# Optimization experiments

Hardware: AMD Instinct MI355X
Metric: run time of the kernel (lower is better)

The kernel has to match this reference:

```python
import jax, jax.numpy as jnp
import numpy as np

K, B, DA = 32, 16384, 128

def setup_inputs() -> dict:
    key = jax.random.key(0)
    ks = jax.random.split(key, 8)
    return {
        "x": jax.random.normal(ks[0], (B, DA), dtype=jnp.float32),
        "neigh_effect": jax.random.uniform(ks[1], (K, B), dtype=jnp.float32),
        "neigh_transform": jax.random.normal(ks[2], (K, B, DA), dtype=jnp.float32),
        "n_param": jax.random.uniform(ks[3], (DA,), dtype=jnp.float32),
        "ew": jax.random.normal(ks[4], (DA,), dtype=jnp.float32) * 0.1,
        "eb": jax.random.normal(ks[5], (1,), dtype=jnp.float32),
        "tw": jax.random.uniform(ks[6], (DA,), dtype=jnp.float32),
        "tb": jax.random.uniform(ks[7], (DA,), dtype=jnp.float32),
    }

def reference(x, neigh_effect, neigh_transform, n_param, ew, eb, tw, tb):
    # x: [B, da] (only used when no neighbors; here K>0 so neighbor path taken)
    k, b = neigh_effect.shape
    da = x.shape[1]
    # softmax over neighbor axis (dim=0 in torch)
    w = jax.nn.softmax(neigh_effect, axis=0)                    # [K, B]
    # faithful to torch reshape trick: x_[i].reshape(da, -1) * w[i], reshape back to (B, da)
    t = neigh_transform.reshape(k, da, b) * w[:, None, :]       # [K, da, B]
    x_sum = t.reshape(k, b, da).sum(axis=0)                     # [B, da]
    x_ = n_param * x_sum                                        # [B, da]
    effect = jax.nn.sigmoid(x_ @ ew + eb)[:, None]              # [B, 1] (Linear(da,1))
    transform = tw * x_ + tb                                    # [B, da]
    return effect, effect * transform
```

## Files before the change

kernel.cpp:

```cpp
#include <hip/hip_runtime.h>
#include <math.h>

#define KN  32
#define BSZ 16384
#define DA  128

__global__ __launch_bounds__(256) void softmax_kernel(const float* __restrict__ ne,
                                                      float* __restrict__ w) {
    const int j = blockIdx.x * 256 + threadIdx.x;
    float v[KN];
    float m = -1e30f;
#pragma unroll
    for (int k = 0; k < KN; ++k) {
        v[k] = ne[k * BSZ + j];
        m = fmaxf(m, v[k]);
    }
    float s = 0.f;
#pragma unroll
    for (int k = 0; k < KN; ++k) {
        v[k] = __expf(v[k] - m);
        s += v[k];
    }
    const float inv = 1.f / s;
#pragma unroll
    for (int k = 0; k < KN; ++k) {
        w[k * BSZ + j] = v[k] * inv;
    }
}

__global__ __launch_bounds__(256) void main_kernel(const float* __restrict__ nt,
                                                   const float* __restrict__ w,
                                                   const float* __restrict__ n_param,
                                                   const float* __restrict__ ew,
                                                   const float* __restrict__ eb,
                                                   const float* __restrict__ tw,
                                                   const float* __restrict__ tb,
                                                   float* __restrict__ out) {
    const int f4 = blockIdx.x * 256 + threadIdx.x;
    const int f  = f4 * 4;
    const int dd = f & (DA - 1);
    const int wj = f & (BSZ - 1);

    float4 acc = make_float4(0.f, 0.f, 0.f, 0.f);
#pragma unroll
    for (int k = 0; k < KN; ++k) {
        const float4 a  = *(const float4*)(nt + (size_t)k * (BSZ * DA) + f);
        const float4 ww = *(const float4*)(w + k * BSZ + wj);
        acc.x += a.x * ww.x;
        acc.y += a.y * ww.y;
        acc.z += a.z * ww.z;
        acc.w += a.w * ww.w;
    }

    const float4 np4 = *(const float4*)(n_param + dd);
    float4 xv;
    xv.x = np4.x * acc.x;
    xv.y = np4.y * acc.y;
    xv.z = np4.z * acc.z;
    xv.w = np4.w * acc.w;

    const float4 ew4 = *(const float4*)(ew + dd);
    float p = xv.x * ew4.x + xv.y * ew4.y + xv.z * ew4.z + xv.w * ew4.w;
    p += __shfl_xor(p, 1);
    p += __shfl_xor(p, 2);
    p += __shfl_xor(p, 4);
    p += __shfl_xor(p, 8);
    p += __shfl_xor(p, 16);

    const float effectv = 1.f / (1.f + __expf(-(p + eb[0])));

    const int bb = f >> 7;
    if ((threadIdx.x & 31) == 0) {
        out[bb] = effectv;
    }

    const float4 tw4 = *(const float4*)(tw + dd);
    const float4 tb4 = *(const float4*)(tb + dd);
    float4 o;
    o.x = effectv * (tw4.x * xv.x + tb4.x);
    o.y = effectv * (tw4.y * xv.y + tb4.y);
    o.z = effectv * (tw4.z * xv.z + tb4.z);
    o.w = effectv * (tw4.w * xv.w + tb4.w);
    *(float4*)(out + BSZ + f) = o;
}

extern "C" void kernel_launch(void* const* d_in, const int* in_sizes, int n_in,
                              void* d_out, int out_size, void* d_ws, size_t ws_size,
                              hipStream_t stream) {
    const float* ne = (const float*)d_in[1];
    const float* nt = (const float*)d_in[2];
    const float* np = (const float*)d_in[3];
    const float* ew = (const float*)d_in[4];
    const float* eb = (const float*)d_in[5];
    const float* tw = (const float*)d_in[6];
    const float* tb = (const float*)d_in[7];
    float* out = (float*)d_out;
    float* w   = (float*)d_ws;

    softmax_kernel<<<BSZ / 256, 256, 0, stream>>>(ne, w);
    main_kernel<<<(BSZ * DA / 4) / 256, 256, 0, stream>>>(nt, w, np, ew, eb, tw, tb, out);
}
```

Baseline: 377.6 us.

## Fuse softmax into main kernel and use nontemporal loads/stores

Removes the separate softmax kernel and its workspace write by recomputing the max, exps and sum inline in the main kernel from neigh_effect. Normalization is deferred to one divide at the end. Streaming neigh_transform loads and output stores now use nontemporal hints to avoid polluting cache. Each element re-reads neigh_effect twice and recomputes exps redundantly across the DA/4 threads sharing the same weights, trading ALU and L2 traffic for one fewer launch.

```diff
diff --git a/kernel.cpp b/kernel.cpp
--- a/kernel.cpp
+++ b/kernel.cpp
@@ -5,61 +5,51 @@
 #define BSZ 16384
 #define DA  128
 
-__global__ __launch_bounds__(256) void softmax_kernel(const float* __restrict__ ne,
-                                                      float* __restrict__ w) {
-    const int j = blockIdx.x * 256 + threadIdx.x;
-    float v[KN];
-    float m = -1e30f;
-#pragma unroll
-    for (int k = 0; k < KN; ++k) {
-        v[k] = ne[k * BSZ + j];
-        m = fmaxf(m, v[k]);
-    }
-    float s = 0.f;
-#pragma unroll
-    for (int k = 0; k < KN; ++k) {
-        v[k] = __expf(v[k] - m);
-        s += v[k];
-    }
-    const float inv = 1.f / s;
-#pragma unroll
-    for (int k = 0; k < KN; ++k) {
-        w[k * BSZ + j] = v[k] * inv;
-    }
-}
+typedef float f32x4 __attribute__((ext_vector_type(4)));
 
-__global__ __launch_bounds__(256) void main_kernel(const float* __restrict__ nt,
-                                                   const float* __restrict__ w,
-                                                   const float* __restrict__ n_param,
-                                                   const float* __restrict__ ew,
-                                                   const float* __restrict__ eb,
-                                                   const float* __restrict__ tw,
-                                                   const float* __restrict__ tb,
-                                                   float* __restrict__ out) {
+__global__ __launch_bounds__(256) void fused_kernel(const float* __restrict__ nt,
+                                                    const float* __restrict__ ne,
+                                                    const float* __restrict__ n_param,
+                                                    const float* __restrict__ ew,
+                                                    const float* __restrict__ eb,
+                                                    const float* __restrict__ tw,
+                                                    const float* __restrict__ tb,
+                                                    float* __restrict__ out) {
     const int f4 = blockIdx.x * 256 + threadIdx.x;
     const int f  = f4 * 4;
     const int dd = f & (DA - 1);
     const int wj = f & (BSZ - 1);
 
-    float4 acc = make_float4(0.f, 0.f, 0.f, 0.f);
+    f32x4 m4 = {-1e30f, -1e30f, -1e30f, -1e30f};
 #pragma unroll
     for (int k = 0; k < KN; ++k) {
-        const float4 a  = *(const float4*)(nt + (size_t)k * (BSZ * DA) + f);
-        const float4 ww = *(const float4*)(w + k * BSZ + wj);
-        acc.x += a.x * ww.x;
-        acc.y += a.y * ww.y;
-        acc.z += a.z * ww.z;
-        acc.w += a.w * ww.w;
+        const f32x4 v = *(const f32x4*)(ne + k * BSZ + wj);
+        m4.x = fmaxf(m4.x, v.x);
+        m4.y = fmaxf(m4.y, v.y);
+        m4.z = fmaxf(m4.z, v.z);
+        m4.w = fmaxf(m4.w, v.w);
     }
 
-    const float4 np4 = *(const float4*)(n_param + dd);
-    float4 xv;
-    xv.x = np4.x * acc.x;
-    xv.y = np4.y * acc.y;
-    xv.z = np4.z * acc.z;
-    xv.w = np4.w * acc.w;
+    f32x4 s4  = {0.f, 0.f, 0.f, 0.f};
+    f32x4 acc = {0.f, 0.f, 0.f, 0.f};
+#pragma unroll
+    for (int k = 0; k < KN; ++k) {
+        const f32x4 v = *(const f32x4*)(ne + k * BSZ + wj);
+        const f32x4 a = __builtin_nontemporal_load(
+            (const f32x4*)(nt + (size_t)k * (BSZ * DA) + f));
+        f32x4 e;
+        e.x = __expf(v.x - m4.x);
+        e.y = __expf(v.y - m4.y);
+        e.z = __expf(v.z - m4.z);
+        e.w = __expf(v.w - m4.w);
+        s4 += e;
+        acc += a * e;
+    }
 
-    const float4 ew4 = *(const float4*)(ew + dd);
+    const f32x4 np4 = *(const f32x4*)(n_param + dd);
+    f32x4 xv = np4 * acc / s4;
+
+    const f32x4 ew4 = *(const f32x4*)(ew + dd);
     float p = xv.x * ew4.x + xv.y * ew4.y + xv.z * ew4.z + xv.w * ew4.w;
     p += __shfl_xor(p, 1);
     p += __shfl_xor(p, 2);
@@ -74,14 +64,10 @@
         out[bb] = effectv;
     }
 
-    const float4 tw4 = *(const float4*)(tw + dd);
-    const float4 tb4 = *(const float4*)(tb + dd);
-    float4 o;
-    o.x = effectv * (tw4.x * xv.x + tb4.x);
-    o.y = effectv * (tw4.y * xv.y + tb4.y);
-    o.z = effectv * (tw4.z * xv.z + tb4.z);
-    o.w = effectv * (tw4.w * xv.w + tb4.w);
-    *(float4*)(out + BSZ + f) = o;
+    const f32x4 tw4 = *(const f32x4*)(tw + dd);
+    const f32x4 tb4 = *(const f32x4*)(tb + dd);
+    f32x4 o = effectv * (tw4 * xv + tb4);
+    __builtin_nontemporal_store(o, (f32x4*)(out + BSZ + f));
 }
 
 extern "C" void kernel_launch(void* const* d_in, const int* in_sizes, int n_in,
@@ -95,8 +81,6 @@
     const float* tw = (const float*)d_in[6];
     const float* tb = (const float*)d_in[7];
     float* out = (float*)d_out;
-    float* w   = (float*)d_ws;
 
-    softmax_kernel<<<BSZ / 256, 256, 0, stream>>>(ne, w);
-    main_kernel<<<(BSZ * DA / 4) / 256, 256, 0, stream>>>(nt, w, np, ew, eb, tw, tb, out);
+    fused_kernel<<<(BSZ * DA / 4) / 256, 256, 0, stream>>>(nt, ne, np, ew, eb, tw, tb, out);
 }
```

New measurement: 362.6 us. 1.04x faster.
